# Kernel tuning notes

Hardware: AMD Instinct MI355X
Metric: run time of the kernel (lower is better)

Reference implementation:

```python
import jax, jax.numpy as jnp
import numpy as np

B, T, H, V = 256, 256, 512, 32000
L = 3  # stacked LSTM layers


def setup_inputs() -> dict:
    key = jax.random.key(0)
    ks = jax.random.split(key, 12)
    s = 0.05
    n = lambda k, shp: (jax.random.normal(k, shp, jnp.float32) * s)
    return {
        "text_1": jax.random.randint(ks[0], (B, T), 0, V, dtype=jnp.int32),
        "text_2": jax.random.randint(ks[1], (B, T), 0, V, dtype=jnp.int32),
        "text_3": jax.random.randint(ks[2], (B, T), 0, V, dtype=jnp.int32),
        "emb": n(ks[3], (V, H)),
        "Wx": n(ks[4], (L, H, 4 * H)),
        "Wh": n(ks[5], (L, H, 4 * H)),
        "b": jnp.zeros((L, 4 * H), jnp.float32),
        "g1": jnp.ones((3 * H,), jnp.float32), "beta1": jnp.zeros((3 * H,), jnp.float32),
        "W1": n(ks[6], (3 * H, 2 * H)), "bd1": jnp.zeros((2 * H,), jnp.float32),
        "g2": jnp.ones((2 * H,), jnp.float32), "beta2": jnp.zeros((2 * H,), jnp.float32),
        "W2": n(ks[7], (2 * H, H // 5)), "bd2": jnp.zeros((H // 5,), jnp.float32),
        "g3": jnp.ones((H // 5,), jnp.float32), "beta3": jnp.zeros((H // 5,), jnp.float32),
        "W3": n(ks[8], (H // 5, 4)), "bd3": jnp.zeros((4,), jnp.float32),
    }


def _lstm_stack(tokens, emb, Wx, Wh, b):
    # tokens: [B, T] int -> last hidden of top layer [B, H]
    x = emb[tokens]                      # [B, T, H]
    x = jnp.transpose(x, (1, 0, 2))      # [T, B, H] (scan over time)
    bsz, h = x.shape[1], Wh.shape[1]
    for l in range(Wx.shape[0]):
        Wx_l, Wh_l, b_l = Wx[l], Wh[l], b[l]
        def step(carry, xt):
            hprev, cprev = carry
            gates = xt @ Wx_l + hprev @ Wh_l + b_l      # [B, 4H]
            i, f, g, o = jnp.split(gates, 4, axis=-1)
            c = jax.nn.sigmoid(f) * cprev + jax.nn.sigmoid(i) * jnp.tanh(g)
            hnew = jax.nn.sigmoid(o) * jnp.tanh(c)
            return (hnew, c), hnew
        init = (jnp.zeros((bsz, h), x.dtype), jnp.zeros((bsz, h), x.dtype))
        _, x = jax.lax.scan(step, init, x)
    return x[-1]                          # rnn_output[:, -1, :]


def _bn(x, gamma, beta, eps=1e-3):
    m = jnp.mean(x, axis=0)
    v = jnp.var(x, axis=0)
    return gamma * (x - m) * jax.lax.rsqrt(v + eps) + beta


def reference(text_1, text_2, text_3, emb, Wx, Wh, b,
              g1, beta1, W1, bd1, g2, beta2, W2, bd2, g3, beta3, W3, bd3):
    r1 = _lstm_stack(text_1, emb, Wx, Wh, b)
    r2 = _lstm_stack(text_2, emb, Wx, Wh, b)
    r3 = _lstm_stack(text_3, emb, Wx, Wh, b)
    r = jnp.concatenate([r1, r2, r3], axis=1)   # [B, 3H]
    r = _bn(r, g1, beta1)
    r = jax.nn.selu(r @ W1 + bd1)
    r = _bn(r, g2, beta2)
    r = jax.nn.selu(r @ W2 + bd2)
    r = _bn(r, g3, beta3)
    return r @ W3 + bd3                          # [B, 4] logits
```

## Files before the change

kernel.cpp:

```cpp
#include <hip/hip_runtime.h>
#include <hip/hip_bf16.h>

typedef __attribute__((ext_vector_type(8))) short short8;
typedef __attribute__((ext_vector_type(4))) float floatx4;

namespace {
constexpr int kB1 = 256;
constexpr int kT  = 256;
constexpr int kH  = 512;
constexpr int kL  = 3;
constexpr int kK  = 1024;
constexpr int kN  = 2048;
constexpr int kGrid = 576;
constexpr size_t kHB = (size_t)768 * kH;

constexpr size_t WREP_OFF   = 0;
constexpr size_t WREP_BYTES = (size_t)kL * kK * kN * 2;
constexpr size_t BREP_OFF   = WREP_OFF + WREP_BYTES;
constexpr size_t BREP_BYTES = (size_t)kL * kN * 4;
constexpr size_t HBUF_OFF   = BREP_OFF + BREP_BYTES;
constexpr size_t HBUF_BYTES = (size_t)kL * 2 * kHB * 2;
constexpr size_t CBUF_OFF   = HBUF_OFF + HBUF_BYTES;
constexpr size_t CBUF_BYTES = (size_t)kL * kHB * 4;
constexpr size_t BNA_OFF    = CBUF_OFF + CBUF_BYTES;
constexpr size_t BNC_OFF    = BNA_OFF + 1536 * 4;
constexpr size_t Z1_OFF     = BNC_OFF + 1536 * 4;
constexpr size_t Z2_OFF     = Z1_OFF + (size_t)256 * 1024 * 4;
constexpr size_t SYNC_OFF   = Z2_OFF + (size_t)256 * 102 * 4;
constexpr int kSyncUints = 32 * 14;
}

__device__ __forceinline__ float ldf(const void* p, size_t idx, int isf32) {
  if (isf32) return ((const float*)p)[idx];
  return __bfloat162float(((const __hip_bfloat16*)p)[idx]);
}

__device__ __forceinline__ short f2bs(float x) {
  union { __hip_bfloat16 h; short s; } u;
  u.h = __float2bfloat16(x);
  return u.s;
}

__device__ __forceinline__ void sync_lds() {
  asm volatile("s_waitcnt lgkmcnt(0)\n\ts_barrier" ::: "memory");
}

__device__ __forceinline__ void gbar(unsigned* line, unsigned target, unsigned want) {
  __syncthreads();
  if (threadIdx.x == 0) {
    __threadfence();
    unsigned old = __hip_atomic_fetch_add(&line[0], 1u, __ATOMIC_ACQ_REL,
                                          __HIP_MEMORY_SCOPE_AGENT);
    if (old == target - 1) {
      __hip_atomic_store(&line[0], 0u, __ATOMIC_RELAXED, __HIP_MEMORY_SCOPE_AGENT);
      __hip_atomic_store(&line[1], want, __ATOMIC_RELEASE, __HIP_MEMORY_SCOPE_AGENT);
    } else {
      while (__hip_atomic_load(&line[1], __ATOMIC_ACQUIRE,
                               __HIP_MEMORY_SCOPE_AGENT) < want)
        __builtin_amdgcn_s_sleep(1);
    }
    __threadfence();
  }
  __syncthreads();
}

__device__ __forceinline__ float fast_tanh(float x) {
  float e = __expf(2.f * x);
  return __fdividef(e - 1.f, e + 1.f);
}
__device__ __forceinline__ float fast_sigmoid(float x) {
  return __fdividef(1.f, 1.f + __expf(-x));
}

__global__ void detect_kernel(const unsigned* __restrict__ g1, unsigned* __restrict__ sync) {
  int i = threadIdx.x;
  for (int j = i; j < kSyncUints; j += 256) sync[j] = 0u;
  if (i == 0) sync[0] = (g1[0] == 0x3F800000u) ? 1u : 0u;
}

__device__ __forceinline__ void repack_body(
    int start, int stride,
    const void* __restrict__ Wx, const void* __restrict__ Wh,
    const void* __restrict__ bias, int isf32,
    __hip_bfloat16* __restrict__ Wrep, float* __restrict__ brep) {
  for (int idx = start; idx < kL * kK * kN; idx += stride) {
    int j  = idx & 7;
    int n2 = (idx >> 3) & (kN - 1);
    int kg = (idx >> 14) & 127;
    int l  = idx >> 21;
    int k  = kg * 8 + j;
    int ntile = n2 >> 7, c = n2 & 127, g = c >> 5, ul = c & 31;
    int u = ntile * 32 + ul;
    int col = g * 512 + u;
    float v;
    if (k < kH) v = ldf(Wx, ((size_t)l * kH + k) * kN + col, isf32);
    else        v = ldf(Wh, ((size_t)l * kH + (k - kH)) * kN + col, isf32);
    Wrep[idx] = __float2bfloat16(v);
    if (kg == 0 && j == 0) brep[l * kN + n2] = ldf(bias, (size_t)l * kN + col, isf32);
  }
}

__global__ __launch_bounds__(256) void repack_kernel(
    const void* __restrict__ Wx, const void* __restrict__ Wh,
    const void* __restrict__ bias, const int* __restrict__ flagp,
    __hip_bfloat16* __restrict__ Wrep, float* __restrict__ brep) {
  repack_body(blockIdx.x * 256 + threadIdx.x, gridDim.x * 256, Wx, Wh, bias, *flagp,
              Wrep, brep);
}

__device__ __forceinline__ void lstm_step(
    int l, int mt, int nt, int t, int isf32,
    const __hip_bfloat16* __restrict__ WB, float bv0, float bv1,
    __hip_bfloat16* __restrict__ hbuf, float* __restrict__ cl,
    const void* __restrict__ emb, const int* __restrict__ txt,
    char* smem) {
  const int tid = threadIdx.x;
  const int lane = tid & 63;
  const int lm = lane & 15, lq = lane >> 4;
  const int arow = tid >> 2;
  const int kc   = tid & 3;
  const int row_g = mt * 64 + arow;
  const int n0w = nt * 128 + (tid >> 6) * 32;

  const void* xsrc;  bool xf32 = false;
  if (l == 0) {
    int tok = txt[t];
    if (isf32) { xsrc = (const void*)((const float*)emb + (size_t)tok * kH); xf32 = true; }
    else         xsrc = (const void*)((const __hip_bfloat16*)emb + (size_t)tok * kH);
  } else {
    const __hip_bfloat16* hIn = hbuf + ((size_t)(l - 1) * 2 + (t & 1)) * kHB;
    xsrc = (const void*)(hIn + (size_t)row_g * kH);
  }
  const __hip_bfloat16* hrow = nullptr;
  if (t > 0) {
    const __hip_bfloat16* hPrev = hbuf + ((size_t)l * 2 + ((t & 1) ^ 1)) * kHB;
    hrow = hPrev + (size_t)row_g * kH;
  }

  const int e_uu = tid & 31;
  const int e_r0 = tid >> 5;

  char* const buf0 = smem;
  char* const buf1 = smem + 16384;
  const int abase = ((arow >> 4) * 256 + kc * 16 + (arow & 15)) * 16;

  short8 av[4];
  short8 bf[4][2];

  auto loadA = [&](int sl) {
    if ((sl >= 4) && (t == 0)) {
      short8 vz = {0, 0, 0, 0, 0, 0, 0, 0};
#pragma unroll
      for (int jj = 0; jj < 4; jj++) av[jj] = vz;
    } else if (sl < 4 && xf32) {
      const float* sf = (const float*)xsrc + sl * 128;
#pragma unroll
      for (int jj = 0; jj < 4; jj++) {
        const float* q = sf + kc * 8 + jj * 32;
        float4 lo = *(const float4*)q;
        float4 hi = *(const float4*)(q + 4);
        short8 v;
        v[0] = f2bs(lo.x); v[1] = f2bs(lo.y); v[2] = f2bs(lo.z); v[3] = f2bs(lo.w);
        v[4] = f2bs(hi.x); v[5] = f2bs(hi.y); v[6] = f2bs(hi.z); v[7] = f2bs(hi.w);
        av[jj] = v;
      }
    } else {
      const __hip_bfloat16* src = (sl < 4)
          ? ((const __hip_bfloat16*)xsrc + sl * 128)
          : (hrow + (sl - 4) * 128);
#pragma unroll
      for (int jj = 0; jj < 4; jj++)
        av[jj] = *(const short8*)(src + kc * 8 + jj * 32);
    }
  };
  auto writeA = [&](char* b) {
#pragma unroll
    for (int jj = 0; jj < 4; jj++)
      *(short8*)(b + abase + jj * 1024) = av[jj];
  };
  auto loadBfrag = [&](int sl, int kk) {
#pragma unroll
    for (int nf = 0; nf < 2; nf++) {
      size_t kg = (size_t)(sl * 16 + kk * 4 + lq);
      bf[kk][nf] = *(const short8*)(WB + (kg * kN + (n0w + nf * 16 + lm)) * 8);
    }
  };

  loadA(0);
#pragma unroll
  for (int kk = 0; kk < 4; kk++) loadBfrag(0, kk);
  writeA(buf0);
  loadA(1);
  float cold[8];
  if (t > 0) {
#pragma unroll
    for (int ii = 0; ii < 8; ii++) {
      int rowf = e_r0 + 8 * ii;
      cold[ii] = cl[(size_t)(mt * 64 + rowf) * kH + nt * 32 + e_uu];
    }
  } else {
#pragma unroll
    for (int ii = 0; ii < 8; ii++) cold[ii] = 0.f;
  }
  sync_lds();

  floatx4 zf = {0.f, 0.f, 0.f, 0.f};
  floatx4 acc[4][2];
#pragma unroll
  for (int a = 0; a < 4; a++)
#pragma unroll
    for (int b = 0; b < 2; b++) acc[a][b] = zf;

#pragma unroll 1
  for (int sl = 0; sl < 8; sl++) {
    char* const cur = (sl & 1) ? buf1 : buf0;
    char* const nxt = (sl & 1) ? buf0 : buf1;
    if (sl < 7) writeA(nxt);
    if (sl < 6) loadA(sl + 2);
#pragma unroll
    for (int kk = 0; kk < 4; kk++) {
      short8 afrag[4];
#pragma unroll
      for (int mf = 0; mf < 4; mf++)
        afrag[mf] = *(const short8*)(cur + (mf * 4 + kk) * 1024 + lane * 16);
#pragma unroll
      for (int mf = 0; mf < 4; mf++)
#pragma unroll
        for (int nf = 0; nf < 2; nf++)
          acc[mf][nf] = __builtin_amdgcn_mfma_f32_16x16x32_bf16(
              afrag[mf], bf[kk][nf], acc[mf][nf], 0, 0, 0);
      if (sl < 7) loadBfrag(sl + 1, kk);
    }
    sync_lds();
  }

#pragma unroll
  for (int mf = 0; mf < 4; mf++)
#pragma unroll
    for (int r = 0; r < 4; r++) {
      acc[mf][0][r] += bv0;
      acc[mf][1][r] += bv1;
    }

  float* gl = (float*)smem;
  {
    const int wv = tid >> 6;
#pragma unroll
    for (int mf = 0; mf < 4; mf++)
#pragma unroll
      for (int nf = 0; nf < 2; nf++)
#pragma unroll
        for (int r = 0; r < 4; r++) {
          int rowf = mf * 16 + lq * 4 + r;
          int uu   = nf * 16 + lm;
          gl[((size_t)wv * 64 + rowf) * 34 + uu] = acc[mf][nf][r];
        }
  }
  sync_lds();

  __hip_bfloat16* hout = hbuf + ((size_t)l * 2 + (t & 1)) * kHB;
#pragma unroll
  for (int ii = 0; ii < 8; ii++) {
    int rowf = e_r0 + 8 * ii;
    int uu = e_uu;
    float gi = fminf(fmaxf(gl[(0 * 64 + rowf) * 34 + uu], -40.f), 40.f);
    float gf = fminf(fmaxf(gl[(1 * 64 + rowf) * 34 + uu], -40.f), 40.f);
    float gG = fminf(fmaxf(gl[(2 * 64 + rowf) * 34 + uu], -40.f), 40.f);
    float go = fminf(fmaxf(gl[(3 * 64 + rowf) * 34 + uu], -40.f), 40.f);
    size_t off = (size_t)(mt * 64 + rowf) * kH + nt * 32 + uu;
    float cn = fast_sigmoid(gf) * cold[ii] + fast_sigmoid(gi) * fast_tanh(gG);
    float hn = fast_sigmoid(go) * fast_tanh(cn);
    cl[off] = cn;
    hout[off] = __float2bfloat16(hn);
  }
}

__global__ __launch_bounds__(256, 3) void persist_kernel(
    const void* __restrict__ Wx, const void* __restrict__ Wh,
    const void* __restrict__ bias, unsigned* __restrict__ sync,
    __hip_bfloat16* __restrict__ Wrep, float* __restrict__ brep,
    __hip_bfloat16* __restrict__ hbuf, float* __restrict__ cbuf,
    const void* __restrict__ emb,
    const int* __restrict__ t1, const int* __restrict__ t2, const int* __restrict__ t3) {
  __shared__ __align__(16) char smem[34816];
  __shared__ int s_tuple;

  const int bid = blockIdx.x;
  const int tid = threadIdx.x;
  const int isf32 = (int)sync[0];

  if (tid == 0) {
    unsigned xcd;
    asm volatile("s_getreg_b32 %0, hwreg(20, 0, 4)" : "=s"(xcd));
    xcd &= 7u;
    int slot = 0;
    for (int off = 0; off < 8; off++) {
      unsigned x = (xcd + off) & 7u;
      unsigned idx = __hip_atomic_fetch_add(&sync[1 + x], 1u, __ATOMIC_RELAXED,
                                            __HIP_MEMORY_SCOPE_AGENT);
      if (idx < 72u) { slot = (int)(x * 72u + idx); break; }
    }
    s_tuple = slot;
  }

  repack_body(bid * 256 + tid, kGrid * 256, Wx, Wh, bias, isf32, Wrep, brep);
  __syncthreads();

  const int slot = s_tuple;
  const int x = slot / 72, i = slot % 72;
  const int l = i / 24;
  const int rem = i % 24;
  const int mt = rem % 12;
  const int nt = x + 8 * (rem / 12);

  gbar(sync + 32 * 13, kGrid, 1u);

  const __hip_bfloat16* const WB = Wrep + (size_t)l * kK * kN;
  float* const cl = cbuf + (size_t)l * kHB;
  const int n0w = nt * 128 + (tid >> 6) * 32;
  const int lm = tid & 15;
  const float bv0 = brep[l * kN + n0w + lm];
  const float bv1 = brep[l * kN + n0w + 16 + lm];

  const int* txt = nullptr;
  if (l == 0) {
    int row_g = mt * 64 + (tid >> 2);
    int ti = row_g >> 8;
    txt = (ti == 0) ? t1 : (ti == 1) ? t2 : t3;
    txt += (row_g & 255) * kT;
  }

  unsigned* const mline = sync + 32 * (1 + mt);
  for (int s = 0; s < kT + kL - 1; s++) {
    const int t = s - l;
    if (t >= 0 && t < kT)
      lstm_step(l, mt, nt, t, isf32, WB, bv0, bv1, hbuf, cl, emb, txt, smem);
    if (s < kT + kL - 2)
      gbar(mline, 48u, (unsigned)(s + 1));
  }
}

__global__ __launch_bounds__(256, 3) void step_kernel(
    int s,
    const __hip_bfloat16* __restrict__ Wrep, const float* __restrict__ brep,
    __hip_bfloat16* __restrict__ hbuf, float* __restrict__ cbuf,
    const void* __restrict__ emb, const int* __restrict__ flagp,
    const int* __restrict__ t1, const int* __restrict__ t2, const int* __restrict__ t3) {
  __shared__ __align__(16) char smem[34816];
  const int bid = blockIdx.x;
  const int l  = bid / 192;
  const int rr = bid % 192;
  const int nt = rr & 15;
  const int mt = rr >> 4;
  const int t = s - l;
  if (t < 0 || t >= kT) return;
  const int isf32 = *flagp;
  const int tid = threadIdx.x;
  const __hip_bfloat16* WB = Wrep + (size_t)l * kK * kN;
  float* cl = cbuf + (size_t)l * kHB;
  const int n0w = nt * 128 + (tid >> 6) * 32;
  const int lm = tid & 15;
  const float bv0 = brep[l * kN + n0w + lm];
  const float bv1 = brep[l * kN + n0w + 16 + lm];
  const int* txt = nullptr;
  if (l == 0) {
    int row_g = mt * 64 + (tid >> 2);
    int ti = row_g >> 8;
    txt = (ti == 0) ? t1 : (ti == 1) ? t2 : t3;
    txt += (row_g & 255) * kT;
  }
  lstm_step(l, mt, nt, t, isf32, WB, bv0, bv1, hbuf, cl, emb, txt, smem);
}

__global__ __launch_bounds__(256) void stats_kernel(
    int ncols, int mode, const void* __restrict__ src,
    const void* __restrict__ gamma, const void* __restrict__ beta,
    const int* __restrict__ flagp, float* __restrict__ bn_a, float* __restrict__ bn_c) {
  int isf32 = *flagp;
  int col = blockIdx.x * 256 + threadIdx.x;
  if (col >= ncols) return;
  float sum = 0.f, ss = 0.f;
  for (int b = 0; b < kB1; b++) {
    float v;
    if (mode == 0) {
      const __hip_bfloat16* h = (const __hip_bfloat16*)src;
      v = __bfloat162float(h[((size_t)((col >> 9) * kB1 + b)) * kH + (col & 511)]);
    } else {
      v = ((const float*)src)[(size_t)b * ncols + col];
    }
    v = fmaxf(-1e15f, fminf(v, 1e15f));
    sum += v; ss += v * v;
  }
  float mean = sum * (1.f / kB1);
  float var  = ss * (1.f / kB1) - mean * mean;
  float a = ldf(gamma, col, isf32) * rsqrtf(var + 1e-3f);
  bn_a[col] = a;
  bn_c[col] = ldf(beta, col, isf32) - mean * a;
}

__global__ __launch_bounds__(256) void headgemm_kernel(
    int Kd, int Nd, int mode, const void* __restrict__ Asrc,
    const float* __restrict__ bn_a, const float* __restrict__ bn_c,
    const void* __restrict__ W, const void* __restrict__ bias,
    const int* __restrict__ flagp, float* __restrict__ out, int do_selu) {
  __shared__ float As[32][65];
  __shared__ float Bs[32][65];
  int isf32 = *flagp;
  int tid = threadIdx.x;
  int bx = blockIdx.x, by = blockIdx.y;
  int tx = tid & 15, ty = tid >> 4;
  float acc[4][4] = {};
  int am = tid & 63, ak = tid >> 6;
  int bk = tid >> 3, bn8 = (tid & 7) * 8;
  for (int ks = 0; ks < Kd; ks += 32) {
    __syncthreads();
    for (int jj = 0; jj < 8; jj++) {
      int kl = ak * 8 + jj;
      int kg = ks + kl;
      int mg = by * 64 + am;
      float v;
      if (mode == 0) {
        const __hip_bfloat16* h = (const __hip_bfloat16*)Asrc;
        v = __bfloat162float(h[((size_t)((kg >> 9) * kB1 + mg)) * kH + (kg & 511)]);
      } else {
        v = ((const float*)Asrc)[(size_t)mg * Kd + kg];
      }
      As[kl][am] = v * bn_a[kg] + bn_c[kg];
    }
    for (int e = 0; e < 8; e++) {
      int col = bx * 64 + bn8 + e;
      Bs[bk][bn8 + e] = (col < Nd) ? ldf(W, (size_t)(ks + bk) * Nd + col, isf32) : 0.f;
    }
    __syncthreads();
    for (int k = 0; k < 32; k++) {
      float ar[4], br[4];
#pragma unroll
      for (int i = 0; i < 4; i++) ar[i] = As[k][ty * 4 + i];
#pragma unroll
      for (int j = 0; j < 4; j++) br[j] = Bs[k][tx * 4 + j];
#pragma unroll
      for (int i = 0; i < 4; i++)
#pragma unroll
        for (int j = 0; j < 4; j++) acc[i][j] += ar[i] * br[j];
    }
  }
  for (int i = 0; i < 4; i++) {
    int row = by * 64 + ty * 4 + i;
    for (int j = 0; j < 4; j++) {
      int col = bx * 64 + tx * 4 + j;
      if (col < Nd) {
        float y = acc[i][j] + ldf(bias, col, isf32);
        if (do_selu)
          y = (y > 0.f) ? 1.0507009873554805f * y
                        : 1.0507009873554805f * 1.6732632423543772f * (__expf(y) - 1.f);
        out[(size_t)row * Nd + col] = y;
      }
    }
  }
}

__global__ __launch_bounds__(256) void final_kernel(
    const float* __restrict__ z2, const float* __restrict__ bn_a, const float* __restrict__ bn_c,
    const void* __restrict__ W3, const void* __restrict__ bd3,
    const int* __restrict__ flagp, void* __restrict__ out) {
  int isf32 = *flagp;
  int b = threadIdx.x;
  float acc[4] = {0.f, 0.f, 0.f, 0.f};
  for (int j = 0; j < 102; j++) {
    float y = z2[b * 102 + j] * bn_a[j] + bn_c[j];
#pragma unroll
    for (int g = 0; g < 4; g++) acc[g] += y * ldf(W3, j * 4 + g, isf32);
  }
#pragma unroll
  for (int g = 0; g < 4; g++) {
    float y = acc[g] + ldf(bd3, g, isf32);
    if (isf32) ((float*)out)[b * 4 + g] = y;
    else ((__hip_bfloat16*)out)[b * 4 + g] = __float2bfloat16(y);
  }
}

extern "C" void kernel_launch(void* const* d_in, const int* in_sizes, int n_in,
                              void* d_out, int out_size, void* d_ws, size_t ws_size,
                              hipStream_t stream) {
  const int* t1 = (const int*)d_in[0];
  const int* t2 = (const int*)d_in[1];
  const int* t3 = (const int*)d_in[2];
  const void* emb = d_in[3];
  const void* Wx  = d_in[4];
  const void* Wh  = d_in[5];
  const void* bb  = d_in[6];
  const void* g1  = d_in[7];
  const void* be1 = d_in[8];
  const void* W1  = d_in[9];
  const void* bd1 = d_in[10];
  const void* g2  = d_in[11];
  const void* be2 = d_in[12];
  const void* W2  = d_in[13];
  const void* bd2 = d_in[14];
  const void* g3  = d_in[15];
  const void* be3 = d_in[16];
  const void* W3  = d_in[17];
  const void* bd3 = d_in[18];

  char* ws = (char*)d_ws;
  __hip_bfloat16* Wrep = (__hip_bfloat16*)(ws + WREP_OFF);
  float* brep = (float*)(ws + BREP_OFF);
  __hip_bfloat16* hbuf = (__hip_bfloat16*)(ws + HBUF_OFF);
  float* cbuf = (float*)(ws + CBUF_OFF);
  float* bn_a = (float*)(ws + BNA_OFF);
  float* bn_c = (float*)(ws + BNC_OFF);
  float* z1 = (float*)(ws + Z1_OFF);
  float* z2 = (float*)(ws + Z2_OFF);
  unsigned* sync = (unsigned*)(ws + SYNC_OFF);
  const int* flag = (const int*)sync;

  detect_kernel<<<1, 256, 0, stream>>>((const unsigned*)g1, sync);

  bool coop_ok = false;
  {
    int numCU = 0, maxBlk = 0;
    int dev = 0;
    if (hipGetDevice(&dev) == hipSuccess &&
        hipDeviceGetAttribute(&numCU, hipDeviceAttributeMultiprocessorCount, dev) == hipSuccess &&
        hipOccupancyMaxActiveBlocksPerMultiprocessor(&maxBlk, (const void*)persist_kernel,
                                                     256, 0) == hipSuccess) {
      if ((long)maxBlk * numCU >= kGrid) {
        void* args[] = {(void*)&Wx, (void*)&Wh, (void*)&bb, (void*)&sync,
                        (void*)&Wrep, (void*)&brep, (void*)&hbuf, (void*)&cbuf,
                        (void*)&emb, (void*)&t1, (void*)&t2, (void*)&t3};
        hipError_t err = hipLaunchCooperativeKernel((const void*)persist_kernel,
                                                    dim3(kGrid), dim3(256), args, 0, stream);
        if (err == hipSuccess) coop_ok = true;
        else (void)hipGetLastError();
      }
    } else {
      (void)hipGetLastError();
    }
  }
  if (!coop_ok) {
    repack_kernel<<<(kL * kK * kN) / 256, 256, 0, stream>>>(Wx, Wh, bb, flag, Wrep, brep);
    for (int s = 0; s < kT + kL - 1; s++)
      step_kernel<<<kGrid, 256, 0, stream>>>(s, Wrep, brep, hbuf, cbuf, emb, flag, t1, t2, t3);
  }

  const __hip_bfloat16* hTop = hbuf + (2 * 2 + 1) * kHB;
  stats_kernel<<<6, 256, 0, stream>>>(1536, 0, hTop, g1, be1, flag, bn_a, bn_c);
  headgemm_kernel<<<dim3(16, 4), 256, 0, stream>>>(1536, 1024, 0, hTop, bn_a, bn_c, W1, bd1, flag, z1, 1);
  stats_kernel<<<4, 256, 0, stream>>>(1024, 1, z1, g2, be2, flag, bn_a, bn_c);
  headgemm_kernel<<<dim3(2, 4), 256, 0, stream>>>(1024, 102, 1, z1, bn_a, bn_c, W2, bd2, flag, z2, 1);
  stats_kernel<<<1, 256, 0, stream>>>(102, 1, z2, g3, be3, flag, bn_a, bn_c);
  final_kernel<<<1, 256, 0, stream>>>(z2, bn_a, bn_c, W3, bd3, flag, (void*)d_out);
}
```

Before: 6.390 ms.

## Relax grid barrier fences, keep LSTM cell state in registers, use coherent h loads

```diff
diff --git a/kernel.cpp b/kernel.cpp
--- a/kernel.cpp
+++ b/kernel.cpp
@@ -35,31 +35,44 @@
   return __bfloat162float(((const __hip_bfloat16*)p)[idx]);
 }
 
-__device__ __forceinline__ short f2bs(float x) {
-  union { __hip_bfloat16 h; short s; } u;
+__device__ __forceinline__ unsigned short f2bs(float x) {
+  union { __hip_bfloat16 h; unsigned short s; } u;
   u.h = __float2bfloat16(x);
   return u.s;
 }
 
 __device__ __forceinline__ void sync_lds() {
   asm volatile("s_waitcnt lgkmcnt(0)\n\ts_barrier" ::: "memory");
+}
+
+__device__ __forceinline__ short8 ld_h16(const __hip_bfloat16* p) {
+  const unsigned long long* q = (const unsigned long long*)p;
+  unsigned long long a = __hip_atomic_load(q,     __ATOMIC_RELAXED, __HIP_MEMORY_SCOPE_AGENT);
+  unsigned long long b = __hip_atomic_load(q + 1, __ATOMIC_RELAXED, __HIP_MEMORY_SCOPE_AGENT);
+  union { unsigned long long u[2]; short8 s; } x;
+  x.u[0] = a; x.u[1] = b;
+  return x.s;
+}
+
+__device__ __forceinline__ void st_h32(__hip_bfloat16* p, unsigned v) {
+  __hip_atomic_store((unsigned*)p, v, __ATOMIC_RELAXED, __HIP_MEMORY_SCOPE_AGENT);
 }
 
 __device__ __forceinline__ void gbar(unsigned* line, unsigned target, unsigned want) {
   __syncthreads();
   if (threadIdx.x == 0) {
-    __threadfence();
-    unsigned old = __hip_atomic_fetch_add(&line[0], 1u, __ATOMIC_ACQ_REL,
+    asm volatile("s_waitcnt vmcnt(0)" ::: "memory");
+    unsigned old = __hip_atomic_fetch_add(&line[0], 1u, __ATOMIC_RELAXED,
                                           __HIP_MEMORY_SCOPE_AGENT);
     if (old == target - 1) {
       __hip_atomic_store(&line[0], 0u, __ATOMIC_RELAXED, __HIP_MEMORY_SCOPE_AGENT);
-      __hip_atomic_store(&line[1], want, __ATOMIC_RELEASE, __HIP_MEMORY_SCOPE_AGENT);
+      asm volatile("s_waitcnt vmcnt(0)" ::: "memory");
+      __hip_atomic_store(&line[1], want, __ATOMIC_RELAXED, __HIP_MEMORY_SCOPE_AGENT);
     } else {
-      while (__hip_atomic_load(&line[1], __ATOMIC_ACQUIRE,
+      while (__hip_atomic_load(&line[1], __ATOMIC_RELAXED,
                                __HIP_MEMORY_SCOPE_AGENT) < want)
-        __builtin_amdgcn_s_sleep(1);
-    }
-    __threadfence();
+        __builtin_amdgcn_s_sleep(2);
+    }
   }
   __syncthreads();
 }
@@ -83,20 +96,29 @@
     const void* __restrict__ Wx, const void* __restrict__ Wh,
     const void* __restrict__ bias, int isf32,
     __hip_bfloat16* __restrict__ Wrep, float* __restrict__ brep) {
-  for (int idx = start; idx < kL * kK * kN; idx += stride) {
+  const int P = kL * kK * kN / 2;
+  for (int p = start; p < P; p += stride) {
+    int idx = p * 2;
     int j  = idx & 7;
     int n2 = (idx >> 3) & (kN - 1);
     int kg = (idx >> 14) & 127;
     int l  = idx >> 21;
-    int k  = kg * 8 + j;
     int ntile = n2 >> 7, c = n2 & 127, g = c >> 5, ul = c & 31;
     int u = ntile * 32 + ul;
     int col = g * 512 + u;
-    float v;
-    if (k < kH) v = ldf(Wx, ((size_t)l * kH + k) * kN + col, isf32);
-    else        v = ldf(Wh, ((size_t)l * kH + (k - kH)) * kN + col, isf32);
-    Wrep[idx] = __float2bfloat16(v);
-    if (kg == 0 && j == 0) brep[l * kN + n2] = ldf(bias, (size_t)l * kN + col, isf32);
+    int k0 = kg * 8 + j;
+    float v0, v1;
+    if (k0 < kH) v0 = ldf(Wx, ((size_t)l * kH + k0) * kN + col, isf32);
+    else         v0 = ldf(Wh, ((size_t)l * kH + (k0 - kH)) * kN + col, isf32);
+    int k1 = k0 + 1;
+    if (k1 < kH) v1 = ldf(Wx, ((size_t)l * kH + k1) * kN + col, isf32);
+    else         v1 = ldf(Wh, ((size_t)l * kH + (k1 - kH)) * kN + col, isf32);
+    unsigned pk = (unsigned)f2bs(v0) | ((unsigned)f2bs(v1) << 16);
+    __hip_atomic_store((unsigned*)(Wrep + idx), pk, __ATOMIC_RELAXED,
+                       __HIP_MEMORY_SCOPE_AGENT);
+    if (kg == 0 && j == 0)
+      __hip_atomic_store(brep + l * kN + n2, ldf(bias, (size_t)l * kN + col, isf32),
+                         __ATOMIC_RELAXED, __HIP_MEMORY_SCOPE_AGENT);
   }
 }
 
@@ -112,6 +134,7 @@
     int l, int mt, int nt, int t, int isf32,
     const __hip_bfloat16* __restrict__ WB, float bv0, float bv1,
     __hip_bfloat16* __restrict__ hbuf, float* __restrict__ cl,
+    float* cold, bool c_in_reg,
     const void* __restrict__ emb, const int* __restrict__ txt,
     char* smem) {
   const int tid = threadIdx.x;
@@ -137,9 +160,6 @@
     hrow = hPrev + (size_t)row_g * kH;
   }
 
-  const int e_uu = tid & 31;
-  const int e_r0 = tid >> 5;
-
   char* const buf0 = smem;
   char* const buf1 = smem + 16384;
   const int abase = ((arow >> 4) * 256 + kc * 16 + (arow & 15)) * 16;
@@ -152,25 +172,37 @@
       short8 vz = {0, 0, 0, 0, 0, 0, 0, 0};
 #pragma unroll
       for (int jj = 0; jj < 4; jj++) av[jj] = vz;
-    } else if (sl < 4 && xf32) {
-      const float* sf = (const float*)xsrc + sl * 128;
-#pragma unroll
-      for (int jj = 0; jj < 4; jj++) {
-        const float* q = sf + kc * 8 + jj * 32;
-        float4 lo = *(const float4*)q;
-        float4 hi = *(const float4*)(q + 4);
-        short8 v;
-        v[0] = f2bs(lo.x); v[1] = f2bs(lo.y); v[2] = f2bs(lo.z); v[3] = f2bs(lo.w);
-        v[4] = f2bs(hi.x); v[5] = f2bs(hi.y); v[6] = f2bs(hi.z); v[7] = f2bs(hi.w);
-        av[jj] = v;
+    } else if (sl < 4) {
+      if (l == 0) {
+        if (xf32) {
+          const float* sf = (const float*)xsrc + sl * 128;
+#pragma unroll
+          for (int jj = 0; jj < 4; jj++) {
+            const float* q = sf + kc * 8 + jj * 32;
+            float4 lo = *(const float4*)q;
+            float4 hi = *(const float4*)(q + 4);
+            short8 v;
+            v[0] = f2bs(lo.x); v[1] = f2bs(lo.y); v[2] = f2bs(lo.z); v[3] = f2bs(lo.w);
+            v[4] = f2bs(hi.x); v[5] = f2bs(hi.y); v[6] = f2bs(hi.z); v[7] = f2bs(hi.w);
+            av[jj] = v;
+          }
+        } else {
+          const __hip_bfloat16* src = (const __hip_bfloat16*)xsrc + sl * 128;
+#pragma unroll
+          for (int jj = 0; jj < 4; jj++)
+            av[jj] = *(const short8*)(src + kc * 8 + jj * 32);
+        }
+      } else {
+        const __hip_bfloat16* src = (const __hip_bfloat16*)xsrc + sl * 128;
+#pragma unroll
+        for (int jj = 0; jj < 4; jj++)
+          av[jj] = ld_h16(src + kc * 8 + jj * 32);
       }
     } else {
-      const __hip_bfloat16* src = (sl < 4)
-          ? ((const __hip_bfloat16*)xsrc + sl * 128)
-          : (hrow + (sl - 4) * 128);
+      const __hip_bfloat16* src = hrow + (sl - 4) * 128;
 #pragma unroll
       for (int jj = 0; jj < 4; jj++)
-        av[jj] = *(const short8*)(src + kc * 8 + jj * 32);
+        av[jj] = ld_h16(src + kc * 8 + jj * 32);
     }
   };
   auto writeA = [&](char* b) {
@@ -191,17 +223,6 @@
   for (int kk = 0; kk < 4; kk++) loadBfrag(0, kk);
   writeA(buf0);
   loadA(1);
-  float cold[8];
-  if (t > 0) {
-#pragma unroll
-    for (int ii = 0; ii < 8; ii++) {
-      int rowf = e_r0 + 8 * ii;
-      cold[ii] = cl[(size_t)(mt * 64 + rowf) * kH + nt * 32 + e_uu];
-    }
-  } else {
-#pragma unroll
-    for (int ii = 0; ii < 8; ii++) cold[ii] = 0.f;
-  }
   sync_lds();
 
   floatx4 zf = {0.f, 0.f, 0.f, 0.f};
@@ -258,20 +279,31 @@
   }
   sync_lds();
 
+  const int e_uu = (tid & 15) * 2;
+  const int e_r0 = tid >> 4;
   __hip_bfloat16* hout = hbuf + ((size_t)l * 2 + (t & 1)) * kHB;
 #pragma unroll
-  for (int ii = 0; ii < 8; ii++) {
-    int rowf = e_r0 + 8 * ii;
-    int uu = e_uu;
-    float gi = fminf(fmaxf(gl[(0 * 64 + rowf) * 34 + uu], -40.f), 40.f);
-    float gf = fminf(fmaxf(gl[(1 * 64 + rowf) * 34 + uu], -40.f), 40.f);
-    float gG = fminf(fmaxf(gl[(2 * 64 + rowf) * 34 + uu], -40.f), 40.f);
-    float go = fminf(fmaxf(gl[(3 * 64 + rowf) * 34 + uu], -40.f), 40.f);
-    size_t off = (size_t)(mt * 64 + rowf) * kH + nt * 32 + uu;
-    float cn = fast_sigmoid(gf) * cold[ii] + fast_sigmoid(gi) * fast_tanh(gG);
-    float hn = fast_sigmoid(go) * fast_tanh(cn);
-    cl[off] = cn;
-    hout[off] = __float2bfloat16(hn);
+  for (int ii = 0; ii < 4; ii++) {
+    int rowf = e_r0 + 16 * ii;
+    float hn2[2];
+#pragma unroll
+    for (int jj = 0; jj < 2; jj++) {
+      int uu = e_uu + jj;
+      float gi = fminf(fmaxf(gl[(0 * 64 + rowf) * 34 + uu], -40.f), 40.f);
+      float gf = fminf(fmaxf(gl[(1 * 64 + rowf) * 34 + uu], -40.f), 40.f);
+      float gG = fminf(fmaxf(gl[(2 * 64 + rowf) * 34 + uu], -40.f), 40.f);
+      float go = fminf(fmaxf(gl[(3 * 64 + rowf) * 34 + uu], -40.f), 40.f);
+      size_t off = (size_t)(mt * 64 + rowf) * kH + nt * 32 + uu;
+      float cprev;
+      if (t == 0) cprev = 0.f;
+      else cprev = c_in_reg ? cold[ii * 2 + jj] : cl[off];
+      float cn = fast_sigmoid(gf) * cprev + fast_sigmoid(gi) * fast_tanh(gG);
+      cold[ii * 2 + jj] = cn;
+      if (!c_in_reg) cl[off] = cn;
+      hn2[jj] = fast_sigmoid(go) * fast_tanh(cn);
+    }
+    unsigned pk = (unsigned)f2bs(hn2[0]) | ((unsigned)f2bs(hn2[1]) << 16);
+    st_h32(hout + (size_t)(mt * 64 + rowf) * kH + nt * 32 + e_uu, pk);
   }
 }
 
@@ -316,7 +348,6 @@
   gbar(sync + 32 * 13, kGrid, 1u);
 
   const __hip_bfloat16* const WB = Wrep + (size_t)l * kK * kN;
-  float* const cl = cbuf + (size_t)l * kHB;
   const int n0w = nt * 128 + (tid >> 6) * 32;
   const int lm = tid & 15;
   const float bv0 = brep[l * kN + n0w + lm];
@@ -330,11 +361,17 @@
     txt += (row_g & 255) * kT;
   }
 
+  float cold[8];
+#pragma unroll
+  for (int q = 0; q < 8; q++) cold[q] = 0.f;
+
   unsigned* const mline = sync + 32 * (1 + mt);
+#pragma unroll 1
   for (int s = 0; s < kT + kL - 1; s++) {
     const int t = s - l;
     if (t >= 0 && t < kT)
-      lstm_step(l, mt, nt, t, isf32, WB, bv0, bv1, hbuf, cl, emb, txt, smem);
+      lstm_step(l, mt, nt, t, isf32, WB, bv0, bv1, hbuf, nullptr, cold, true,
+                emb, txt, smem);
     if (s < kT + kL - 2)
       gbar(mline, 48u, (unsigned)(s + 1));
   }
@@ -369,7 +406,9 @@
     txt = (ti == 0) ? t1 : (ti == 1) ? t2 : t3;
     txt += (row_g & 255) * kT;
   }
-  lstm_step(l, mt, nt, t, isf32, WB, bv0, bv1, hbuf, cl, emb, txt, smem);
+  float cold[8];
+  lstm_step(l, mt, nt, t, isf32, WB, bv0, bv1, hbuf, cl, cold, false,
+            emb, txt, smem);
 }
 
 __global__ __launch_bounds__(256) void stats_kernel(
@@ -538,7 +577,8 @@
     }
   }
   if (!coop_ok) {
-    repack_kernel<<<(kL * kK * kN) / 256, 256, 0, stream>>>(Wx, Wh, bb, flag, Wrep, brep);
+    repack_kernel<<<(kL * kK * kN / 2 + 255) / 256, 256, 0, stream>>>(Wx, Wh, bb, flag,
+                                                                      Wrep, brep);
     for (int s = 0; s < kT + kL - 1; s++)
       step_kernel<<<kGrid, 256, 0, stream>>>(s, Wrep, brep, hbuf, cbuf, emb, flag, t1, t2, t3);
   }
```

Result: slower. 7.966 ms (+24.7%).
